# Kernel optimization log

Measured on AMD Instinct MI355X. Metric: run time of the kernel, lower is better.

Reference implementation:

```python
import jax, jax.numpy as jnp
import numpy as np

H = 1024
L = 4

def _lstm_layer(xs, w_ih, w_hh, b):
    # xs: [B, T, in]; w_ih: [4H, in]; w_hh: [4H, H]; b: [4H] (b_ih + b_hh)
    xp = jnp.einsum('bti,gi->btg', xs, w_ih) + b  # [B, T, 4H]
    xp = jnp.swapaxes(xp, 0, 1)                   # [T, B, 4H]
    B = xs.shape[0]
    h0 = jnp.zeros((B, H), xs.dtype)
    c0 = jnp.zeros((B, H), xs.dtype)

    def step(carry, xp_t):
        h, c = carry
        gates = xp_t + h @ w_hh.T                 # [B, 4H]
        i, f, g, o = jnp.split(gates, 4, axis=-1)  # PyTorch gate order i,f,g,o
        i = jax.nn.sigmoid(i)
        f = jax.nn.sigmoid(f)
        g = jnp.tanh(g)
        o = jax.nn.sigmoid(o)
        c = f * c + i * g
        h = o * jnp.tanh(c)
        return (h, c), h

    (hT, cT), hs = jax.lax.scan(step, (h0, c0), xp)
    return jnp.swapaxes(hs, 0, 1), hT             # [B, T, H], [B, H]


def setup_inputs() -> dict:
    key = jax.random.key(0)
    ks = jax.random.split(key, 8)
    s = 1.0 / np.sqrt(H)
    u = lambda k, shp: jax.random.uniform(k, shp, jnp.float32, -s, s)
    return {
        'x': jax.random.normal(ks[0], (64, 256, 2), jnp.float32),
        'w_ih0': u(ks[1], (4 * H, 2)),            # layer 0 input weights
        'w_ih_rest': u(ks[2], (L - 1, 4 * H, H)), # layers 1..3 input weights
        'w_hh': u(ks[3], (L, 4 * H, H)),
        'b_ih': u(ks[4], (L, 4 * H)),
        'b_hh': u(ks[5], (L, 4 * H)),
        'fc_w': u(ks[6], (1, H)),
        'fc_b': u(ks[7], (1,)),
    }


def reference(x, w_ih0, w_ih_rest, w_hh, b_ih, b_hh, fc_w, fc_b):
    # 4-layer LSTM, batch_first, zero initial states; dropout inactive (eval mode).
    hs, hT = _lstm_layer(x, w_ih0, w_hh[0], b_ih[0] + b_hh[0])
    for l in range(1, L):
        hs, hT = _lstm_layer(hs, w_ih_rest[l - 1], w_hh[l], b_ih[l] + b_hh[l])
    # fc applied to final hidden state of last layer
    return hT @ fc_w.T + fc_b                      # [B, 1]
```

## Files before the change

kernel.cpp:

```cpp
#include <hip/hip_runtime.h>
#include <hip/hip_bf16.h>
#include <hip/hip_fp16.h>


#define H      1024
#define BATCH  64
#define T      256
#define RINGN  8

typedef _Float16 f16x8 __attribute__((ext_vector_type(8)));
typedef _Float16 f16x4 __attribute__((ext_vector_type(4)));
typedef float    f32x4 __attribute__((ext_vector_type(4)));

#define WPACK_HH_SZ  (4ull*64*32*4*64*8*2)
#define WPACK_IH_SZ  (3ull*64*32*4*64*8*2)
#define HRING_OFF    (WPACK_HH_SZ + WPACK_IH_SZ)
#define SLOT_ELEMS   65536
#define SLOT_BYTES   131072ull
#define CNT_INTS     (4*257*16)
#define CNT_BYTES    ((unsigned long long)CNT_INTS*4)

__host__ __device__ __forceinline__ unsigned long long ring_bytes(int nslot) {
  return 4ull*(unsigned)nslot*SLOT_BYTES;
}
__device__ __forceinline__ int cidx(int l, int s) { return (l*257 + s)*16; }

__device__ __forceinline__ int aslot(int s, int fresh) {
  if (!fresh) return s & 7;
  return (s >= 256) ? 256 : (int)(__brev((unsigned)s) >> 24);
}

__device__ __forceinline__ void wait_eq64(int* p) {
  int it = 0;
  while (__hip_atomic_load(p, __ATOMIC_RELAXED, __HIP_MEMORY_SCOPE_AGENT) < 64) {
    __builtin_amdgcn_s_sleep(1);
    if (++it > 100000000) break;
  }
}

__device__ __forceinline__ f16x8 load_h8_sc(const _Float16* p) {
  const unsigned long long* q = (const unsigned long long*)p;
  unsigned long long lo = __hip_atomic_load(q,     __ATOMIC_RELAXED, __HIP_MEMORY_SCOPE_AGENT);
  unsigned long long hi = __hip_atomic_load(q + 1, __ATOMIC_RELAXED, __HIP_MEMORY_SCOPE_AGENT);
  union { unsigned long long u[2]; f16x8 v; } c;
  c.u[0] = lo; c.u[1] = hi;
  return c.v;
}

__global__ void pack_kernel(const float* __restrict__ w_ih_rest,
                            const float* __restrict__ w_hh,
                            char* __restrict__ ws, int nslot)
{
  const long long NS_HH = 4ll*64*32*4*64;
  const long long NS_IH = 3ll*64*32*4*64;
  const long long NS_HZ = 4ll*8192;
  const long long NTOT  = NS_HH + NS_IH + NS_HZ + 4;
  _Float16* whh_dst = (_Float16*)ws;
  _Float16* wih_dst = (_Float16*)(ws + WPACK_HH_SZ);
  int* cnt = (int*)(ws + HRING_OFF + ring_bytes(nslot));
  for (long long i = blockIdx.x*(long long)blockDim.x + threadIdx.x; i < NTOT;
       i += (long long)gridDim.x*blockDim.x) {
    if (i < NS_HH + NS_IH) {
      const bool is_hh = (i < NS_HH);
      long long slot = is_hh ? i : (i - NS_HH);
      long long j = slot;
      int lane = (int)(j & 63); j >>= 6;
      int nt   = (int)(j & 3);  j >>= 2;
      int ks   = (int)(j & 31); j >>= 5;
      int wg   = (int)(j & 63); j >>= 6;
      int l    = (int)j;
      int row = nt*1024 + wg*16 + (lane & 15);
      int col = ks*32 + (lane >> 4)*8;
      const float* src = (is_hh ? w_hh : w_ih_rest) + ((long long)l*4096 + row)*1024 + col;
      f16x8 v;
      #pragma unroll
      for (int e = 0; e < 8; e++) v[e] = (_Float16)src[e];
      *(f16x8*)((is_hh ? whh_dst : wih_dst) + slot*8) = v;
    } else if (i < NS_HH + NS_IH + NS_HZ) {
      long long j = i - (NS_HH + NS_IH);
      long long l = j >> 13;
      long long off = j & 8191;
      uint4 z = make_uint4(0,0,0,0);
      ((uint4*)(ws + HRING_OFF))[(l*(long long)nslot)*8192 + off] = z;
    } else {
      int l = (int)(i - (NS_HH + NS_IH + NS_HZ));
      cnt[cidx(l,0)] = 64;
    }
  }
}

__global__ __launch_bounds__(256, 1) void lstm_main(
    const float* __restrict__ x,
    const float* __restrict__ wih0,
    const float* __restrict__ bih,
    const float* __restrict__ bhh,
    char* __restrict__ ws, int nslot, int fresh)
{
  __builtin_amdgcn_fence(__ATOMIC_ACQUIRE, "agent");

  extern __shared__ char lds[];
  _Float16* whh_lds = (_Float16*)lds;
  _Float16* buf0    = (_Float16*)(lds + 131072);
  _Float16* buf1    = (_Float16*)(lds + 139264);

  const int l   = blockIdx.x >> 6;
  const int wg  = blockIdx.x & 63;
  const int tid = threadIdx.x;
  const int wave = tid >> 6;
  const int lane = tid & 63;

  const _Float16* wpack_hh = (const _Float16*)ws + (size_t)(l*64 + wg)*65536;
  const _Float16* wpack_ih = (l > 0)
      ? (const _Float16*)(ws + WPACK_HH_SZ) + (size_t)((l-1)*64 + wg)*65536
      : wpack_hh;
  _Float16* hring = (_Float16*)(ws + HRING_OFF);
  int* cnt  = (int*)(ws + HRING_OFF + ring_bytes(nslot));
  int* cnt2 = cnt + CNT_INTS;

  {
    const uint4* src = (const uint4*)wpack_hh;
    uint4* dst = (uint4*)whh_lds;
    for (int i = tid; i < 8192; i += 256) dst[i] = src[i];
  }

  const int b_ew = tid >> 2;
  const int u0   = (tid & 3) * 4;
  float cst[4] = {0.f, 0.f, 0.f, 0.f};
  float bias[4][4];
  float wx0[4][4], wx1[4][4];
  #pragma unroll
  for (int ii = 0; ii < 4; ii++) {
    #pragma unroll
    for (int g = 0; g < 4; g++) {
      int row = g*1024 + wg*16 + u0 + ii;
      bias[ii][g] = bih[l*4096 + row] + bhh[l*4096 + row];
      if (l == 0) { wx0[ii][g] = wih0[row*2]; wx1[ii][g] = wih0[row*2 + 1]; }
      else        { wx0[ii][g] = 0.f;         wx1[ii][g] = 0.f; }
    }
  }
  __syncthreads();

  const int m_row = lane & 15, quad = lane >> 4;

  for (int s = 1; s <= T; s++) {
    if (tid == 0)          wait_eq64(&cnt[cidx(l, s-1)]);
    else if (tid == 64)  { if (l > 0) wait_eq64(&cnt[cidx(l-1, s)]); }
    else if (tid == 128) { if (!fresh && l < 3 && s > RINGN) wait_eq64(&cnt2[cidx(l, s-RINGN)]); }
    __syncthreads();

    const _Float16* asrc = (l > 0 && wave < 2)
        ? hring + ((size_t)(l-1)*nslot + aslot(s,   fresh))*SLOT_ELEMS
        : hring + ((size_t)l*nslot     + aslot(s-1, fresh))*SLOT_ELEMS;

    f32x4 acc[4][4];
    #pragma unroll
    for (int mt = 0; mt < 4; mt++)
      #pragma unroll
      for (int nt = 0; nt < 4; nt++) acc[mt][nt] = (f32x4){0.f, 0.f, 0.f, 0.f};

    auto kbody = [&](int ks, bool from_lds, bool plain) {
      const int kb = ks*32 + quad*8;
      f16x8 a[4], bb[4];
      #pragma unroll
      for (int mt = 0; mt < 4; mt++) {
        const _Float16* ap = asrc + (size_t)(mt*16 + m_row)*1024 + kb;
        a[mt] = plain ? *(const f16x8*)ap : load_h8_sc(ap);
      }
      if (from_lds) {
        #pragma unroll
        for (int nt = 0; nt < 4; nt++)
          bb[nt] = *(const f16x8*)(whh_lds + ((ks*4 + nt)*64 + lane)*8);
      } else {
        #pragma unroll
        for (int nt = 0; nt < 4; nt++)
          bb[nt] = *(const f16x8*)(wpack_ih + ((size_t)(ks*4 + nt)*64 + lane)*8);
      }
      #pragma unroll
      for (int mt = 0; mt < 4; mt++)
        #pragma unroll
        for (int nt = 0; nt < 4; nt++)
          acc[mt][nt] = __builtin_amdgcn_mfma_f32_16x16x32_f16(a[mt], bb[nt], acc[mt][nt], 0, 0, 0);
    };

    if (fresh) {
      if (l == 0) {
        #pragma unroll 2
        for (int i = 0; i < 8; i++) kbody(wave*8 + i, true, true);
      } else if (wave < 2) {
        #pragma unroll 2
        for (int i = 0; i < 16; i++) kbody(wave*16 + i, false, true);
      } else {
        #pragma unroll 2
        for (int i = 0; i < 16; i++) kbody((wave-2)*16 + i, true, true);
      }
    } else {
      if (l == 0) {
        #pragma unroll 2
        for (int i = 0; i < 8; i++) kbody(wave*8 + i, true, false);
      } else if (wave < 2) {
        #pragma unroll 2
        for (int i = 0; i < 16; i++) kbody(wave*16 + i, false, false);
      } else {
        #pragma unroll 2
        for (int i = 0; i < 16; i++) kbody((wave-2)*16 + i, true, false);
      }
    }

    _Float16* mybuf = ((wave & 1) == 0) ? buf0 : buf1;
    if (wave >= 2) {
      #pragma unroll
      for (int mt = 0; mt < 4; mt++)
        #pragma unroll
        for (int nt = 0; nt < 4; nt++) {
          f16x4 v;
          #pragma unroll
          for (int e = 0; e < 4; e++) v[e] = (_Float16)acc[mt][nt][e];
          *(f16x4*)(mybuf + ((mt*4 + nt)*64 + lane)*4) = v;
        }
    }
    __syncthreads();
    if (wave < 2) {
      #pragma unroll
      for (int mt = 0; mt < 4; mt++)
        #pragma unroll
        for (int nt = 0; nt < 4; nt++) {
          f16x4 p = *(f16x4*)(mybuf + ((mt*4 + nt)*64 + lane)*4);
          f16x4 v;
          #pragma unroll
          for (int e = 0; e < 4; e++) v[e] = (_Float16)(acc[mt][nt][e] + (float)p[e]);
          *(f16x4*)(mybuf + ((mt*4 + nt)*64 + lane)*4) = v;
        }
    }
    if (!fresh && tid == 0 && l > 0)
      __hip_atomic_fetch_add(&cnt2[cidx(l-1, s)], 1, __ATOMIC_RELAXED, __HIP_MEMORY_SCOPE_AGENT);
    __syncthreads();

    {
      const int mt = b_ew >> 4, q = (b_ew & 15) >> 2, reg = b_ew & 3;
      float xs0 = 0.f, xs1 = 0.f;
      if (l == 0) {
        xs0 = x[((size_t)b_ew*T + (s-1))*2];
        xs1 = x[((size_t)b_ew*T + (s-1))*2 + 1];
      }
      f16x4 hv;
      #pragma unroll
      for (int ii = 0; ii < 4; ii++) {
        const int u = u0 + ii;
        float pre[4];
        #pragma unroll
        for (int g = 0; g < 4; g++) {
          int idx = ((mt*4 + g)*64 + (u + 16*q))*4 + reg;
          pre[g] = (float)buf0[idx] + (float)buf1[idx] + bias[ii][g]
                 + wx0[ii][g]*xs0 + wx1[ii][g]*xs1;
        }
        float ig = 1.f/(1.f + __expf(-pre[0]));
        float fg = 1.f/(1.f + __expf(-pre[1]));
        float gg = 2.f/(1.f + __expf(-2.f*pre[2])) - 1.f;
        float og = 1.f/(1.f + __expf(-pre[3]));
        float c  = fg*cst[ii] + ig*gg;
        cst[ii] = c;
        float th = 2.f/(1.f + __expf(-2.f*c)) - 1.f;
        hv[ii] = (_Float16)(og*th);
      }
      _Float16* hdst = hring + ((size_t)l*nslot + aslot(s, fresh))*SLOT_ELEMS
                     + (size_t)b_ew*1024 + wg*16 + u0;
      union { f16x4 v; unsigned long long u; } cv; cv.v = hv;
      __hip_atomic_store((unsigned long long*)hdst, cv.u,
                         __ATOMIC_RELAXED, __HIP_MEMORY_SCOPE_AGENT);
    }
    __syncthreads();
    if (tid == 0)
      __hip_atomic_fetch_add(&cnt[cidx(l, s)], 1, __ATOMIC_RELAXED, __HIP_MEMORY_SCOPE_AGENT);
  }
}

__global__ void fc_kernel(const char* __restrict__ ws,
                          const float* __restrict__ fcw,
                          const float* __restrict__ fcb,
                          float* __restrict__ out, int nslot, int fresh)
{
  const _Float16* h3 = (const _Float16*)(ws + HRING_OFF)
                     + ((size_t)3*nslot + aslot(T, fresh))*SLOT_ELEMS;
  __shared__ float red[256];
  const int tid = threadIdx.x;
  const int b = tid >> 2, p = tid & 3;
  float sum = 0.f;
  for (int j = p*256; j < p*256 + 256; j++)
    sum += fcw[j] * (float)h3[(size_t)b*1024 + j];
  red[tid] = sum;
  __syncthreads();
  if (p == 0)
    out[b] = red[tid] + red[tid+1] + red[tid+2] + red[tid+3] + fcb[0];
}

extern "C" void kernel_launch(void* const* d_in, const int* in_sizes, int n_in,
                              void* d_out, int out_size, void* d_ws, size_t ws_size,
                              hipStream_t stream)
{
  const float* x    = (const float*)d_in[0];
  const float* wih0 = (const float*)d_in[1];
  const float* wihr = (const float*)d_in[2];
  const float* whh  = (const float*)d_in[3];
  const float* bih  = (const float*)d_in[4];
  const float* bhh  = (const float*)d_in[5];
  const float* fcw  = (const float*)d_in[6];
  const float* fcb  = (const float*)d_in[7];
  float* out = (float*)d_out;
  char* ws = (char*)d_ws;
  (void)in_sizes; (void)n_in; (void)out_size;

  const unsigned long long ws_big   = HRING_OFF + ring_bytes(257) + 2*CNT_BYTES;
  const unsigned long long ws_small = HRING_OFF + ring_bytes(8)   + 2*CNT_BYTES;
  if (ws_size < ws_small) return;
  const int fresh = (ws_size >= ws_big) ? 1 : 0;
  const int nslot = fresh ? 257 : 8;

  hipFuncSetAttribute(reinterpret_cast<const void*>(lstm_main),
                      hipFuncAttributeMaxDynamicSharedMemorySize, 147456);

  hipMemsetAsync(ws + HRING_OFF + ring_bytes(nslot), 0, (size_t)(2*CNT_BYTES), stream);
  pack_kernel<<<512, 256, 0, stream>>>(wihr, whh, ws, nslot);
  lstm_main<<<256, 256, 147456, stream>>>(x, wih0, bih, bhh, ws, nslot, fresh);
  fc_kernel<<<1, 256, 0, stream>>>(ws, fcw, fcb, out, nslot, fresh);
}
```

Before: 4.067 ms.

## Keep per-wave weight slices resident in registers instead of LDS/global

Each wave now loads its slice of the packed recurrent or input weights once into a 64-entry f16x8 register array and reuses it every timestep. This removes the per-step LDS weight reads and, for layers above 0, the per-step global reads of input weights. The partial-sum exchange buffers also move from fp16 to fp32, which keeps more precision in the split-K reduction, and LDS use shrinks to 32KB. The risk is very high VGPR pressure (about 256 registers just for weights), which could cause spills that wipe out the gain.

New measurement: 5.278 ms. +29.8%, slower.

```diff
diff --git a/kernel.cpp b/kernel.cpp
--- a/kernel.cpp
+++ b/kernel.cpp
@@ -99,9 +99,8 @@
   __builtin_amdgcn_fence(__ATOMIC_ACQUIRE, "agent");
 
   extern __shared__ char lds[];
-  _Float16* whh_lds = (_Float16*)lds;
-  _Float16* buf0    = (_Float16*)(lds + 131072);
-  _Float16* buf1    = (_Float16*)(lds + 139264);
+  float* buf0 = (float*)lds;
+  float* buf1 = (float*)(lds + 16384);
 
   const int l   = blockIdx.x >> 6;
   const int wg  = blockIdx.x & 63;
@@ -117,10 +116,23 @@
   int* cnt  = (int*)(ws + HRING_OFF + ring_bytes(nslot));
   int* cnt2 = cnt + CNT_INTS;
 
+  const int ksb = (l == 0) ? wave*8 : (wave & 1)*16;
+  f16x8 bc[64];
   {
-    const uint4* src = (const uint4*)wpack_hh;
-    uint4* dst = (uint4*)whh_lds;
-    for (int i = tid; i < 8192; i += 256) dst[i] = src[i];
+    const _Float16* bsrc = (l > 0 && wave < 2) ? wpack_ih : wpack_hh;
+    if (l == 0) {
+      #pragma unroll
+      for (int i = 0; i < 8; i++)
+        #pragma unroll
+        for (int nt = 0; nt < 4; nt++)
+          bc[i*4+nt] = *(const f16x8*)(bsrc + ((size_t)((ksb+i)*4 + nt)*64 + lane)*8);
+    } else {
+      #pragma unroll
+      for (int i = 0; i < 16; i++)
+        #pragma unroll
+        for (int nt = 0; nt < 4; nt++)
+          bc[i*4+nt] = *(const f16x8*)(bsrc + ((size_t)((ksb+i)*4 + nt)*64 + lane)*8);
+    }
   }
 
   const int b_ew = tid >> 2;
@@ -138,7 +150,6 @@
       else        { wx0[ii][g] = 0.f;         wx1[ii][g] = 0.f; }
     }
   }
-  __syncthreads();
 
   const int m_row = lane & 15, quad = lane >> 4;
 
@@ -158,65 +169,46 @@
       #pragma unroll
       for (int nt = 0; nt < 4; nt++) acc[mt][nt] = (f32x4){0.f, 0.f, 0.f, 0.f};
 
-    auto kbody = [&](int ks, bool from_lds, bool plain) {
-      const int kb = ks*32 + quad*8;
-      f16x8 a[4], bb[4];
+    auto kbody = [&](int i, bool plain) {
+      const int kb = (ksb + i)*32 + quad*8;
+      f16x8 a[4];
       #pragma unroll
       for (int mt = 0; mt < 4; mt++) {
         const _Float16* ap = asrc + (size_t)(mt*16 + m_row)*1024 + kb;
         a[mt] = plain ? *(const f16x8*)ap : load_h8_sc(ap);
       }
-      if (from_lds) {
+      #pragma unroll
+      for (int mt = 0; mt < 4; mt++)
         #pragma unroll
         for (int nt = 0; nt < 4; nt++)
-          bb[nt] = *(const f16x8*)(whh_lds + ((ks*4 + nt)*64 + lane)*8);
-      } else {
-        #pragma unroll
-        for (int nt = 0; nt < 4; nt++)
-          bb[nt] = *(const f16x8*)(wpack_ih + ((size_t)(ks*4 + nt)*64 + lane)*8);
-      }
-      #pragma unroll
-      for (int mt = 0; mt < 4; mt++)
-        #pragma unroll
-        for (int nt = 0; nt < 4; nt++)
-          acc[mt][nt] = __builtin_amdgcn_mfma_f32_16x16x32_f16(a[mt], bb[nt], acc[mt][nt], 0, 0, 0);
+          acc[mt][nt] = __builtin_amdgcn_mfma_f32_16x16x32_f16(a[mt], bc[i*4+nt], acc[mt][nt], 0, 0, 0);
     };
 
     if (fresh) {
       if (l == 0) {
-        #pragma unroll 2
-        for (int i = 0; i < 8; i++) kbody(wave*8 + i, true, true);
-      } else if (wave < 2) {
-        #pragma unroll 2
-        for (int i = 0; i < 16; i++) kbody(wave*16 + i, false, true);
+        #pragma unroll
+        for (int i = 0; i < 8; i++) kbody(i, true);
       } else {
-        #pragma unroll 2
-        for (int i = 0; i < 16; i++) kbody((wave-2)*16 + i, true, true);
+        #pragma unroll
+        for (int i = 0; i < 16; i++) kbody(i, true);
       }
     } else {
       if (l == 0) {
-        #pragma unroll 2
-        for (int i = 0; i < 8; i++) kbody(wave*8 + i, true, false);
-      } else if (wave < 2) {
-        #pragma unroll 2
-        for (int i = 0; i < 16; i++) kbody(wave*16 + i, false, false);
+        #pragma unroll
+        for (int i = 0; i < 8; i++) kbody(i, false);
       } else {
-        #pragma unroll 2
-        for (int i = 0; i < 16; i++) kbody((wave-2)*16 + i, true, false);
-      }
-    }
-
-    _Float16* mybuf = ((wave & 1) == 0) ? buf0 : buf1;
+        #pragma unroll
+        for (int i = 0; i < 16; i++) kbody(i, false);
+      }
+    }
+
+    float* mybuf = ((wave & 1) == 0) ? buf0 : buf1;
     if (wave >= 2) {
       #pragma unroll
       for (int mt = 0; mt < 4; mt++)
         #pragma unroll
-        for (int nt = 0; nt < 4; nt++) {
-          f16x4 v;
-          #pragma unroll
-          for (int e = 0; e < 4; e++) v[e] = (_Float16)acc[mt][nt][e];
-          *(f16x4*)(mybuf + ((mt*4 + nt)*64 + lane)*4) = v;
-        }
+        for (int nt = 0; nt < 4; nt++)
+          *(f32x4*)(mybuf + ((mt*4 + nt)*64 + lane)*4) = acc[mt][nt];
     }
     __syncthreads();
     if (wave < 2) {
@@ -224,11 +216,8 @@
       for (int mt = 0; mt < 4; mt++)
         #pragma unroll
         for (int nt = 0; nt < 4; nt++) {
-          f16x4 p = *(f16x4*)(mybuf + ((mt*4 + nt)*64 + lane)*4);
-          f16x4 v;
-          #pragma unroll
-          for (int e = 0; e < 4; e++) v[e] = (_Float16)(acc[mt][nt][e] + (float)p[e]);
-          *(f16x4*)(mybuf + ((mt*4 + nt)*64 + lane)*4) = v;
+          f32x4 p = *(f32x4*)(mybuf + ((mt*4 + nt)*64 + lane)*4);
+          *(f32x4*)(mybuf + ((mt*4 + nt)*64 + lane)*4) = acc[mt][nt] + p;
         }
     }
     if (!fresh && tid == 0 && l > 0)
@@ -250,7 +239,7 @@
         #pragma unroll
         for (int g = 0; g < 4; g++) {
           int idx = ((mt*4 + g)*64 + (u + 16*q))*4 + reg;
-          pre[g] = (float)buf0[idx] + (float)buf1[idx] + bias[ii][g]
+          pre[g] = buf0[idx] + buf1[idx] + bias[ii][g]
                  + wx0[ii][g]*xs0 + wx1[ii][g]*xs1;
         }
         float ig = 1.f/(1.f + __expf(-pre[0]));
@@ -316,10 +305,10 @@
   const int nslot = fresh ? 257 : 8;
 
   hipFuncSetAttribute(reinterpret_cast<const void*>(lstm_main),
-                      hipFuncAttributeMaxDynamicSharedMemorySize, 147456);
+                      hipFuncAttributeMaxDynamicSharedMemorySize, 32768);
 
   hipMemsetAsync(ws + HRING_OFF + ring_bytes(nslot), 0, (size_t)(2*CNT_BYTES), stream);
   pack_kernel<<<512, 256, 0, stream>>>(wihr, whh, ws, nslot);
-  lstm_main<<<256, 256, 147456, stream>>>(x, wih0, bih, bhh, ws, nslot, fresh);
+  lstm_main<<<256, 256, 32768, stream>>>(x, wih0, bih, bhh, ws, nslot, fresh);
   fc_kernel<<<1, 256, 0, stream>>>(ws, fcw, fcb, out, nslot, fresh);
 }
```

## Cache input-projection weights in registers and split both GEMMs evenly across waves

Applied to the files above, without the earlier changes.

For layers above the first, each wave now loads its 8-kstep slice of the packed input-to-hidden weights into registers once, before the time loop. Every wave then runs 8 input-projection ksteps and 8 recurrent ksteps per timestep. Before, two waves streamed the input weights from global memory on every step while the other two handled the recurrent part from LDS. This removes the per-step global weight reloads and balances the work across waves, at the cost of 128 extra VGPRs per lane, which risks spills or lower occupancy. The input term for layer 0 is also guarded so it only runs when l==0.

New measurement: 4.859 ms. 1.19x slower.

```diff
diff --git a/kernel.cpp b/kernel.cpp
--- a/kernel.cpp
+++ b/kernel.cpp
@@ -123,6 +123,16 @@
     for (int i = tid; i < 8192; i += 256) dst[i] = src[i];
   }
 
+  const int ksb = wave*8;
+  f16x8 bc[32];
+  if (l > 0) {
+    #pragma unroll
+    for (int i = 0; i < 8; i++)
+      #pragma unroll
+      for (int nt = 0; nt < 4; nt++)
+        bc[i*4+nt] = *(const f16x8*)(wpack_ih + ((size_t)((ksb+i)*4 + nt)*64 + lane)*8);
+  }
+
   const int b_ew = tid >> 2;
   const int u0   = (tid & 3) * 4;
   float cst[4] = {0.f, 0.f, 0.f, 0.f};
@@ -135,7 +145,6 @@
       int row = g*1024 + wg*16 + u0 + ii;
       bias[ii][g] = bih[l*4096 + row] + bhh[l*4096 + row];
       if (l == 0) { wx0[ii][g] = wih0[row*2]; wx1[ii][g] = wih0[row*2 + 1]; }
-      else        { wx0[ii][g] = 0.f;         wx1[ii][g] = 0.f; }
     }
   }
   __syncthreads();
@@ -148,9 +157,11 @@
     else if (tid == 128) { if (!fresh && l < 3 && s > RINGN) wait_eq64(&cnt2[cidx(l, s-RINGN)]); }
     __syncthreads();
 
-    const _Float16* asrc = (l > 0 && wave < 2)
+    const _Float16* asrc_ih = (l > 0)
         ? hring + ((size_t)(l-1)*nslot + aslot(s,   fresh))*SLOT_ELEMS
-        : hring + ((size_t)l*nslot     + aslot(s-1, fresh))*SLOT_ELEMS;
+        : (const _Float16*)nullptr;
+    const _Float16* asrc_hh =
+          hring + ((size_t)l*nslot     + aslot(s-1, fresh))*SLOT_ELEMS;
 
     f32x4 acc[4][4];
     #pragma unroll
@@ -158,23 +169,32 @@
       #pragma unroll
       for (int nt = 0; nt < 4; nt++) acc[mt][nt] = (f32x4){0.f, 0.f, 0.f, 0.f};
 
-    auto kbody = [&](int ks, bool from_lds, bool plain) {
+    auto kbody_ih = [&](int i, bool plain) {
+      const int kb = (ksb + i)*32 + quad*8;
+      f16x8 a[4];
+      #pragma unroll
+      for (int mt = 0; mt < 4; mt++) {
+        const _Float16* ap = asrc_ih + (size_t)(mt*16 + m_row)*1024 + kb;
+        a[mt] = plain ? *(const f16x8*)ap : load_h8_sc(ap);
+      }
+      #pragma unroll
+      for (int mt = 0; mt < 4; mt++)
+        #pragma unroll
+        for (int nt = 0; nt < 4; nt++)
+          acc[mt][nt] = __builtin_amdgcn_mfma_f32_16x16x32_f16(a[mt], bc[i*4+nt], acc[mt][nt], 0, 0, 0);
+    };
+    auto kbody_hh = [&](int i, bool plain) {
+      const int ks = ksb + i;
       const int kb = ks*32 + quad*8;
       f16x8 a[4], bb[4];
       #pragma unroll
       for (int mt = 0; mt < 4; mt++) {
-        const _Float16* ap = asrc + (size_t)(mt*16 + m_row)*1024 + kb;
+        const _Float16* ap = asrc_hh + (size_t)(mt*16 + m_row)*1024 + kb;
         a[mt] = plain ? *(const f16x8*)ap : load_h8_sc(ap);
       }
-      if (from_lds) {
-        #pragma unroll
-        for (int nt = 0; nt < 4; nt++)
-          bb[nt] = *(const f16x8*)(whh_lds + ((ks*4 + nt)*64 + lane)*8);
-      } else {
-        #pragma unroll
-        for (int nt = 0; nt < 4; nt++)
-          bb[nt] = *(const f16x8*)(wpack_ih + ((size_t)(ks*4 + nt)*64 + lane)*8);
-      }
+      #pragma unroll
+      for (int nt = 0; nt < 4; nt++)
+        bb[nt] = *(const f16x8*)(whh_lds + ((ks*4 + nt)*64 + lane)*8);
       #pragma unroll
       for (int mt = 0; mt < 4; mt++)
         #pragma unroll
@@ -183,27 +203,19 @@
     };
 
     if (fresh) {
-      if (l == 0) {
+      if (l > 0) {
         #pragma unroll 2
-        for (int i = 0; i < 8; i++) kbody(wave*8 + i, true, true);
-      } else if (wave < 2) {
+        for (int i = 0; i < 8; i++) kbody_ih(i, true);
+      }
+      #pragma unroll 2
+      for (int i = 0; i < 8; i++) kbody_hh(i, true);
+    } else {
+      if (l > 0) {
         #pragma unroll 2
-        for (int i = 0; i < 16; i++) kbody(wave*16 + i, false, true);
-      } else {
-        #pragma unroll 2
-        for (int i = 0; i < 16; i++) kbody((wave-2)*16 + i, true, true);
-      }
-    } else {
-      if (l == 0) {
-        #pragma unroll 2
-        for (int i = 0; i < 8; i++) kbody(wave*8 + i, true, false);
-      } else if (wave < 2) {
-        #pragma unroll 2
-        for (int i = 0; i < 16; i++) kbody(wave*16 + i, false, false);
-      } else {
-        #pragma unroll 2
-        for (int i = 0; i < 16; i++) kbody((wave-2)*16 + i, true, false);
-      }
+        for (int i = 0; i < 8; i++) kbody_ih(i, false);
+      }
+      #pragma unroll 2
+      for (int i = 0; i < 8; i++) kbody_hh(i, false);
     }
 
     _Float16* mybuf = ((wave & 1) == 0) ? buf0 : buf1;
@@ -237,12 +249,12 @@
 
     {
       const int mt = b_ew >> 4, q = (b_ew & 15) >> 2, reg = b_ew & 3;
+      f16x4 hv;
       float xs0 = 0.f, xs1 = 0.f;
       if (l == 0) {
         xs0 = x[((size_t)b_ew*T + (s-1))*2];
         xs1 = x[((size_t)b_ew*T + (s-1))*2 + 1];
       }
-      f16x4 hv;
       #pragma unroll
       for (int ii = 0; ii < 4; ii++) {
         const int u = u0 + ii;
@@ -250,8 +262,8 @@
         #pragma unroll
         for (int g = 0; g < 4; g++) {
           int idx = ((mt*4 + g)*64 + (u + 16*q))*4 + reg;
-          pre[g] = (float)buf0[idx] + (float)buf1[idx] + bias[ii][g]
-                 + wx0[ii][g]*xs0 + wx1[ii][g]*xs1;
+          pre[g] = (float)buf0[idx] + (float)buf1[idx] + bias[ii][g];
+          if (l == 0) pre[g] += wx0[ii][g]*xs0 + wx1[ii][g]*xs1;
         }
         float ig = 1.f/(1.f + __expf(-pre[0]));
         float fg = 1.f/(1.f + __expf(-pre[1]));
```
